# Kernel optimization log

Measured on AMD Instinct MI355X. Metric: run time of the kernel, lower is better.

The kernel has to match this reference:

```python
import jax, jax.numpy as jnp
import numpy as np

N_Q = 8          # number of residual quantizer stages
N_CODES = 1024   # 2 ** (75 // N_q + 1)
D = 128
GAMMA = 0.99


def setup_inputs() -> dict:
    key = jax.random.key(0)
    k1, k2, k3, k4 = jax.random.split(key, 4)
    data_object = jax.random.normal(k1, (16, D, 2048), dtype=jnp.float32)
    weights = jax.random.normal(k2, (N_Q, N_CODES, D), dtype=jnp.float32)
    # EMA cluster-size buffer; scale so most codes are 'alive' (>= 2)
    N_i = jax.random.uniform(k3, (N_Q, N_CODES), dtype=jnp.float32) * 100.0
    m_i = jax.random.normal(k4, (N_Q, N_CODES, D), dtype=jnp.float32)
    return {"data_object": data_object, "weights": weights, "N_i": N_i, "m_i": m_i}


def reference(data_object, weights, N_i, m_i):
    b, d, s = data_object.shape
    y = jnp.transpose(data_object, (0, 2, 1))  # [b, s, D]
    residual = y
    cur_y = jnp.zeros_like(y)
    all_idx, new_Ni, new_mi, new_W = [], [], [], []
    key = jax.random.key(42)
    one_m_g = 1.0 - GAMMA
    for i in range(N_Q):
        W = weights[i]  # [N, D]
        # squared euclidean distances: ||y||^2 + ||W||^2 - 2 y.W^T  -> [b, s, N]
        dist = ((residual ** 2).sum(-1)[..., None]
                + (W ** 2).sum(-1)[None, None, :]
                - 2.0 * jnp.einsum('bsd,nd->bsn', residual, W))
        idx = jnp.argmin(dist, axis=-1)          # [b, s]
        Q = W[idx]                               # gather  [b, s, D]
        cur_y = cur_y + Q
        flat_idx = idx.reshape(-1)               # [b*s]
        flat_res = residual.reshape(-1, d)       # [b*s, D]
        # fused scatter-reduce replacing the torch per-code mask loop
        counts = jax.ops.segment_sum(jnp.ones(flat_idx.shape, jnp.float32),
                                     flat_idx, num_segments=N_CODES)
        sums = jax.ops.segment_sum(flat_res, flat_idx, num_segments=N_CODES)
        Ni_new = N_i[i] * GAMMA + counts * one_m_g
        mi_new = m_i[i] * GAMMA + sums * one_m_g
        w_new = mi_new / jnp.clip(Ni_new, 1e-8)[:, None]
        # dead-code replacement with random residual vectors
        dead = Ni_new < 2.0
        rid = jax.random.randint(jax.random.fold_in(key, i), (N_CODES,),
                                 0, flat_res.shape[0])
        w_new = jnp.where(dead[:, None], flat_res[rid], w_new)
        all_idx.append(idx)
        new_Ni.append(Ni_new)
        new_mi.append(mi_new)
        new_W.append(w_new)
        residual = residual - Q
    cur_y_t = jnp.transpose(cur_y, (0, 2, 1))  # [b, D, s]
    # straight-through estimator
    logits = data_object + jax.lax.stop_gradient(cur_y_t - data_object)
    commitment_loss = jnp.mean((jax.lax.stop_gradient(cur_y_t) - data_object) ** 2)
    indices = jnp.stack(all_idx, axis=0)  # [N_q, b, s]
    return (logits, commitment_loss, indices,
            jnp.stack(new_Ni), jnp.stack(new_mi), jnp.stack(new_W))
```

## Files before the change

### kernel.cpp

```cpp
#include <hip/hip_runtime.h>
#include <hip/hip_bf16.h>

#define NQ 8
#define NC 1024
#define DD 128
#define BB 16
#define SS 2048
#define RR (BB * SS)
#define GAMMA_F 0.99f
#define TAU 0.03f

typedef __attribute__((ext_vector_type(8))) short bf16x8;
typedef __attribute__((ext_vector_type(4))) float f32x4;

typedef __attribute__((address_space(3))) void lds_void;
typedef const __attribute__((address_space(1))) void g1_void;
__device__ __forceinline__ void gload16(const void* g, void* l) {
  __builtin_amdgcn_global_load_lds((g1_void*)g, (lds_void*)l, 16, 0, 0);
}

__device__ __forceinline__ ushort f2bf(float x) {
  __hip_bfloat16 b = __float2bfloat16(x);
  return *reinterpret_cast<ushort*>(&b);
}
__device__ __forceinline__ float bf2f(ushort u) {
  unsigned v = ((unsigned)u) << 16;
  return *reinterpret_cast<float*>(&v);
}

__device__ __forceinline__ int swz(int r) {
  return ((r & 7) << 2) | ((r >> 3) & 1);
}

__global__ __launch_bounds__(256) void k_transpose_in(
    const float* __restrict__ data, float* __restrict__ res)
{
  __shared__ float tile[32][33];
  int b = blockIdx.z;
  int s0 = blockIdx.x << 5, d0 = blockIdx.y << 5;
  int tx = threadIdx.x, ty = threadIdx.y;
  #pragma unroll
  for (int r = 0; r < 32; r += 8)
    tile[ty + r][tx] = data[((size_t)b * DD + d0 + ty + r) * SS + s0 + tx];
  __syncthreads();
  #pragma unroll
  for (int r = 0; r < 32; r += 8)
    res[((size_t)b * SS + s0 + ty + r) * DD + d0 + tx] = tile[tx][ty + r];
}

__global__ void k_wsq(const float* __restrict__ W, float* __restrict__ wsq)
{
  int c = blockIdx.x * blockDim.x + threadIdx.x;
  if (c >= NQ * NC) return;
  const float4* p = reinterpret_cast<const float4*>(W + (size_t)c * DD);
  float s = 0.f;
  #pragma unroll 8
  for (int k = 0; k < DD / 4; ++k) {
    float4 v = p[k];
    s += v.x * v.x + v.y * v.y + v.z * v.z + v.w * v.w;
  }
  wsq[c] = s;
}

__global__ __launch_bounds__(256) void k_split(
    const float* __restrict__ src, ushort* __restrict__ dst)
{
  int fi = blockIdx.x * 256 + threadIdx.x;
  const float4* sp = reinterpret_cast<const float4*>(src) + (size_t)fi * 2;
  float4 a = sp[0], b = sp[1];
  ushort4 h0, h1, l0, l1;
  h0.x = f2bf(a.x); l0.x = f2bf(a.x - bf2f(h0.x));
  h0.y = f2bf(a.y); l0.y = f2bf(a.y - bf2f(h0.y));
  h0.z = f2bf(a.z); l0.z = f2bf(a.z - bf2f(h0.z));
  h0.w = f2bf(a.w); l0.w = f2bf(a.w - bf2f(h0.w));
  h1.x = f2bf(b.x); l1.x = f2bf(b.x - bf2f(h1.x));
  h1.y = f2bf(b.y); l1.y = f2bf(b.y - bf2f(h1.y));
  h1.z = f2bf(b.z); l1.z = f2bf(b.z - bf2f(h1.z));
  h1.w = f2bf(b.w); l1.w = f2bf(b.w - bf2f(h1.w));
  ushort4* dp = reinterpret_cast<ushort4*>(dst + (size_t)fi * 16);
  dp[0] = h0; dp[1] = h1; dp[2] = l0; dp[3] = l1;
}

__global__ __launch_bounds__(512, 2) void k_argmin(
    const ushort* __restrict__ res_hl, const ushort* __restrict__ w_hl,
    const float* __restrict__ wsq,
    int* __restrict__ idxw, float* __restrict__ idxf,
    int* __restrict__ count, int* __restrict__ fb_count,
    int* __restrict__ fb_list, int stage)
{
  __shared__ bf16x8 Bs[2][2048];
  __shared__ float Lm1[4][64], Lm2[4][64];
  __shared__ int   Li1[4][64];

  const int t = threadIdx.x;
  const int l = t & 63;
  const int w = t >> 6;
  const int wm = w >> 2;
  const int wn = w & 3;
  const int row0 = blockIdx.x * 64;
  const int l15 = l & 15, kg = l >> 4;
  const float* wsqs = wsq + stage * NC;

  bf16x8 ah[2][4], al[2][4];
  #pragma unroll
  for (int mf = 0; mf < 2; ++mf) {
    int r = row0 + wm * 32 + mf * 16 + l15;
    const bf16x8* rowp = reinterpret_cast<const bf16x8*>(res_hl + (size_t)r * 256);
    #pragma unroll
    for (int ks = 0; ks < 4; ++ks) {
      int ch = ks * 8 + kg * 2;
      ah[mf][ks] = rowp[ch];
      al[mf][ks] = rowp[ch + 1];
    }
  }

  #pragma unroll
  for (int it = 0; it < 4; ++it) {
    int fi = it * 512 + t;
    int cr = fi >> 5, sc = fi & 31;
    gload16(w_hl + ((size_t)(stage * NC + cr) * 32 + (sc ^ swz(cr))) * 8, &Bs[0][fi]);
  }
  #pragma unroll
  for (int it = 0; it < 4; ++it) {
    int fi = it * 512 + t;
    int cr = fi >> 5, sc = fi & 31;
    gload16(w_hl + ((size_t)(stage * NC + 64 + cr) * 32 + (sc ^ swz(cr))) * 8, &Bs[1][fi]);
  }

  float m1[2][4], m2[2][4];
  int i1[2][4];
  #pragma unroll
  for (int mf = 0; mf < 2; ++mf)
    #pragma unroll
    for (int rg = 0; rg < 4; ++rg) { m1[mf][rg] = 3.4e38f; m2[mf][rg] = 3.4e38f; i1[mf][rg] = 0; }

  for (int ct = 0; ct < 16; ++ct) {
    if (ct < 15) asm volatile("s_waitcnt vmcnt(4)" ::: "memory");
    else         asm volatile("s_waitcnt vmcnt(0)" ::: "memory");
    __builtin_amdgcn_sched_barrier(0);
    __builtin_amdgcn_s_barrier();

    const bf16x8* Bb = Bs[ct & 1];
    const int cr = wn * 16 + l15;

    f32x4 zero = {0.f, 0.f, 0.f, 0.f};
    f32x4 acc[2];
    acc[0] = zero; acc[1] = zero;

    #pragma unroll
    for (int ks = 0; ks < 4; ++ks) {
      const int ch = ks * 8 + kg * 2;
      bf16x8 bh = Bb[cr * 32 + (ch ^ swz(cr))];
      bf16x8 bl = Bb[cr * 32 + ((ch + 1) ^ swz(cr))];
      #pragma unroll
      for (int mf = 0; mf < 2; ++mf) {
        f32x4 cc = acc[mf];
        cc = __builtin_amdgcn_mfma_f32_16x16x32_bf16(ah[mf][ks], bh, cc, 0, 0, 0);
        cc = __builtin_amdgcn_mfma_f32_16x16x32_bf16(al[mf][ks], bh, cc, 0, 0, 0);
        cc = __builtin_amdgcn_mfma_f32_16x16x32_bf16(ah[mf][ks], bl, cc, 0, 0, 0);
        acc[mf] = cc;
      }
    }

    {
      int code = ct * 64 + wn * 16 + l15;
      float sq = wsqs[code];
      #pragma unroll
      for (int mf = 0; mf < 2; ++mf)
        #pragma unroll
        for (int rg = 0; rg < 4; ++rg) {
          float s = fmaf(-2.f, acc[mf][rg], sq);
          if (s < m1[mf][rg]) { m2[mf][rg] = m1[mf][rg]; m1[mf][rg] = s; i1[mf][rg] = code; }
          else if (s < m2[mf][rg]) m2[mf][rg] = s;
        }
    }

    __builtin_amdgcn_sched_barrier(0);
    __builtin_amdgcn_s_barrier();
    if (ct + 2 < 16) {
      bf16x8* dst = Bs[ct & 1];
      #pragma unroll
      for (int it = 0; it < 4; ++it) {
        int fi = it * 512 + t;
        int cr2 = fi >> 5, sc = fi & 31;
        gload16(w_hl + ((size_t)(stage * NC + (ct + 2) * 64 + cr2) * 32 + (sc ^ swz(cr2))) * 8,
                &dst[fi]);
      }
    }
  }

  #pragma unroll
  for (int mk = 1; mk <= 8; mk <<= 1) {
    #pragma unroll
    for (int mf = 0; mf < 2; ++mf)
      #pragma unroll
      for (int rg = 0; rg < 4; ++rg) {
        float om1 = __shfl_xor(m1[mf][rg], mk);
        int   oi  = __shfl_xor(i1[mf][rg], mk);
        float om2 = __shfl_xor(m2[mf][rg], mk);
        bool bwin = (om1 < m1[mf][rg]) || (om1 == m1[mf][rg] && oi < i1[mf][rg]);
        float lose = bwin ? m1[mf][rg] : om1;
        m2[mf][rg] = fminf(fminf(m2[mf][rg], om2), lose);
        if (bwin) { m1[mf][rg] = om1; i1[mf][rg] = oi; }
      }
  }
  if (l15 == 0) {
    #pragma unroll
    for (int mf = 0; mf < 2; ++mf)
      #pragma unroll
      for (int rg = 0; rg < 4; ++rg) {
        int rl = wm * 32 + mf * 16 + kg * 4 + rg;
        Lm1[wn][rl] = m1[mf][rg];
        Lm2[wn][rl] = m2[mf][rg];
        Li1[wn][rl] = i1[mf][rg];
      }
  }
  __syncthreads();

  if (t < 64) {
    float gm1 = Lm1[0][t], gm2 = Lm2[0][t];
    int gi = Li1[0][t];
    #pragma unroll
    for (int q = 1; q < 4; ++q) {
      float b1 = Lm1[q][t], b2 = Lm2[q][t];
      int bi = Li1[q][t];
      bool bwin = (b1 < gm1) || (b1 == gm1 && bi < gi);
      float lose = bwin ? gm1 : b1;
      gm2 = fminf(fminf(gm2, b2), lose);
      if (bwin) { gm1 = b1; gi = bi; }
    }
    int row = row0 + t;
    if (gm2 - gm1 > TAU) {
      idxw[row] = gi;
      idxf[row] = (float)gi;
      atomicAdd(&count[gi], 1);
    } else {
      int p = atomicAdd(fb_count, 1);
      fb_list[p] = row;
    }
  }
}

__global__ __launch_bounds__(256) void k_fallback(
    const float* __restrict__ res, const float* __restrict__ W,
    const float* __restrict__ wsq, const int* __restrict__ fb_count,
    const int* __restrict__ fb_list,
    int* __restrict__ idxw, float* __restrict__ idxf,
    int* __restrict__ count, int stage)
{
  __shared__ float rr[128];
  __shared__ float sv[256];
  __shared__ int   si[256];
  int n = *fb_count;
  int t = threadIdx.x;
  for (int b = blockIdx.x; b < n; b += gridDim.x) {
    int row = fb_list[b];
    __syncthreads();
    if (t < 128) rr[t] = res[(size_t)row * DD + t];
    __syncthreads();
    float bm = 3.4e38f; int bi = 0;
    #pragma unroll
    for (int j = 0; j < 4; ++j) {
      int c = t + j * 256;
      const float4* wp = reinterpret_cast<const float4*>(W + ((size_t)stage * NC + c) * DD);
      float dot = 0.f;
      #pragma unroll 8
      for (int k = 0; k < 32; ++k) {
        float4 wv = wp[k];
        dot = fmaf(rr[4 * k + 0], wv.x, dot);
        dot = fmaf(rr[4 * k + 1], wv.y, dot);
        dot = fmaf(rr[4 * k + 2], wv.z, dot);
        dot = fmaf(rr[4 * k + 3], wv.w, dot);
      }
      float s = fmaf(-2.f, dot, wsq[stage * NC + c]);
      if (s < bm || (s == bm && c < bi)) { bm = s; bi = c; }
    }
    sv[t] = bm; si[t] = bi;
    __syncthreads();
    for (int sft = 128; sft > 0; sft >>= 1) {
      if (t < sft) {
        float ov = sv[t + sft]; int oi = si[t + sft];
        if (ov < sv[t] || (ov == sv[t] && oi < si[t])) { sv[t] = ov; si[t] = oi; }
      }
      __syncthreads();
    }
    if (t == 0) {
      int win = si[0];
      idxw[row] = win;
      idxf[row] = (float)win;
      atomicAdd(&count[win], 1);
    }
  }
}

__global__ __launch_bounds__(1024) void k_scan(
    int* __restrict__ count, int* __restrict__ offs, int* __restrict__ pos)
{
  __shared__ int sc[1024];
  int t = threadIdx.x;
  sc[t] = count[t];
  __syncthreads();
  for (int off = 1; off < 1024; off <<= 1) {
    int v = (t >= off) ? sc[t - off] : 0;
    __syncthreads();
    sc[t] += v;
    __syncthreads();
  }
  offs[t + 1] = sc[t];
  if (t == 0) { offs[0] = 0; count[1024] = 0; }
  pos[t] = 0;
  count[t] = 0;
}

__global__ __launch_bounds__(256) void k_scatter(
    const int* __restrict__ idxw, const int* __restrict__ offs,
    int* __restrict__ pos, int* __restrict__ rows_sorted)
{
  int r = blockIdx.x * 256 + threadIdx.x;
  int c = idxw[r];
  int slot = offs[c] + atomicAdd(&pos[c], 1);
  rows_sorted[slot] = r;
}

__device__ __forceinline__ unsigned rotl32(unsigned v, int r) { return (v << r) | (v >> (32 - r)); }

__device__ void threefry2x32(unsigned ks0, unsigned ks1, unsigned x0, unsigned x1,
                             unsigned& o0, unsigned& o1)
{
  unsigned ks2 = ks0 ^ ks1 ^ 0x1BD11BDAu;
  x0 += ks0; x1 += ks1;
  x0 += x1; x1 = rotl32(x1, 13); x1 ^= x0;
  x0 += x1; x1 = rotl32(x1, 15); x1 ^= x0;
  x0 += x1; x1 = rotl32(x1, 26); x1 ^= x0;
  x0 += x1; x1 = rotl32(x1, 6);  x1 ^= x0;
  x0 += ks1; x1 += ks2 + 1u;
  x0 += x1; x1 = rotl32(x1, 17); x1 ^= x0;
  x0 += x1; x1 = rotl32(x1, 29); x1 ^= x0;
  x0 += x1; x1 = rotl32(x1, 16); x1 ^= x0;
  x0 += x1; x1 = rotl32(x1, 24); x1 ^= x0;
  x0 += ks2; x1 += ks0 + 2u;
  x0 += x1; x1 = rotl32(x1, 13); x1 ^= x0;
  x0 += x1; x1 = rotl32(x1, 15); x1 ^= x0;
  x0 += x1; x1 = rotl32(x1, 26); x1 ^= x0;
  x0 += x1; x1 = rotl32(x1, 6);  x1 ^= x0;
  x0 += ks0; x1 += ks1 + 3u;
  x0 += x1; x1 = rotl32(x1, 17); x1 ^= x0;
  x0 += x1; x1 = rotl32(x1, 29); x1 ^= x0;
  x0 += x1; x1 = rotl32(x1, 16); x1 ^= x0;
  x0 += x1; x1 = rotl32(x1, 24); x1 ^= x0;
  x0 += ks1; x1 += ks2 + 4u;
  x0 += x1; x1 = rotl32(x1, 13); x1 ^= x0;
  x0 += x1; x1 = rotl32(x1, 15); x1 ^= x0;
  x0 += x1; x1 = rotl32(x1, 26); x1 ^= x0;
  x0 += x1; x1 = rotl32(x1, 6);  x1 ^= x0;
  x0 += ks2; x1 += ks0 + 5u;
  o0 = x0; o1 = x1;
}

__global__ __launch_bounds__(1024) void k_finalize(
    const float* __restrict__ Ni_in, const float* __restrict__ mi_in,
    const int* __restrict__ offs, const int* __restrict__ rows_sorted,
    const float* __restrict__ res_cur,
    float* __restrict__ outNi, float* __restrict__ outmi, float* __restrict__ outW,
    int stage)
{
  __shared__ float red[8][128];
  const float ONEMG = (float)(1.0 - 0.99);
  int c = blockIdx.x;
  int t = threadIdx.x;
  int d = t & 127;
  int jw = t >> 7;
  int base = offs[c];
  int cnt = offs[c + 1] - base;
  const int* rs = rows_sorted + base;

  float sum = 0.f;
  int j = jw;
  for (; j + 24 < cnt; j += 32) {
    int r0 = rs[j];
    int r1 = rs[j + 8];
    int r2 = rs[j + 16];
    int r3 = rs[j + 24];
    float v0 = res_cur[(size_t)r0 * DD + d];
    float v1 = res_cur[(size_t)r1 * DD + d];
    float v2 = res_cur[(size_t)r2 * DD + d];
    float v3 = res_cur[(size_t)r3 * DD + d];
    sum += v0 + v1 + v2 + v3;
  }
  for (; j < cnt; j += 8)
    sum += res_cur[(size_t)rs[j] * DD + d];

  red[jw][d] = sum;
  __syncthreads();

  if (jw == 0) {
    float s = red[0][d] + red[1][d] + red[2][d] + red[3][d]
            + red[4][d] + red[5][d] + red[6][d] + red[7][d];
    float ni = Ni_in[stage * NC + c] * GAMMA_F + (float)cnt * ONEMG;
    float mm = mi_in[((size_t)stage * NC + c) * DD + d] * GAMMA_F + s * ONEMG;
    float w = mm / fmaxf(ni, 1e-8f);
    if (ni < 2.0f) {
      unsigned K0, K1, a0, a1, b0, b1, o0, o1;
      threefry2x32(0u, 42u, 0u, (unsigned)stage, K0, K1);
      threefry2x32(K0, K1, 0u, 2u, a0, a1);
      threefry2x32(K0, K1, 1u, 3u, b0, b1);
      unsigned bits;
      if (c < 512) { threefry2x32(a1, b1, (unsigned)c, (unsigned)(c + 512), o0, o1); bits = o0; }
      else         { threefry2x32(a1, b1, (unsigned)(c - 512), (unsigned)c, o0, o1); bits = o1; }
      int rid = (int)(bits & 32767u);
      w = res_cur[(size_t)rid * DD + d];
    }
    if (d == 0) outNi[stage * NC + c] = ni;
    size_t o = ((size_t)stage * NC + c) * DD + d;
    outmi[o] = mm;
    outW[o] = w;
  }
}

__global__ __launch_bounds__(256) void k_update(
    float* __restrict__ res, const float* __restrict__ W,
    const int* __restrict__ idx, ushort* __restrict__ res_hl, int stage)
{
  int row = blockIdx.x * 8 + (threadIdx.x >> 5);
  int d4 = threadIdx.x & 31;
  int id = idx[row];
  float4 r = reinterpret_cast<const float4*>(res + (size_t)row * DD)[d4];
  float4 q = reinterpret_cast<const float4*>(W + ((size_t)stage * NC + id) * DD)[d4];
  float4 o;
  o.x = r.x - q.x; o.y = r.y - q.y; o.z = r.z - q.z; o.w = r.w - q.w;
  reinterpret_cast<float4*>(res + (size_t)row * DD)[d4] = o;
  ushort4 hi, lo;
  hi.x = f2bf(o.x); lo.x = f2bf(o.x - bf2f(hi.x));
  hi.y = f2bf(o.y); lo.y = f2bf(o.y - bf2f(hi.y));
  hi.z = f2bf(o.z); lo.z = f2bf(o.z - bf2f(hi.z));
  hi.w = f2bf(o.w); lo.w = f2bf(o.w - bf2f(hi.w));
  size_t g = ((size_t)row * 16 + (d4 >> 1)) * 2;
  *reinterpret_cast<ushort4*>(res_hl + g * 8 + (d4 & 1) * 4) = hi;
  *reinterpret_cast<ushort4*>(res_hl + (g + 1) * 8 + (d4 & 1) * 4) = lo;
}

__global__ __launch_bounds__(256) void k_final(
    const float* __restrict__ data, const float* __restrict__ res,
    float* __restrict__ logits, float* __restrict__ partials)
{
  __shared__ float tile[32][33];
  __shared__ float wsum[4];
  int b = blockIdx.z, s0 = blockIdx.x << 5, d0 = blockIdx.y << 5;
  int tx = threadIdx.x, ty = threadIdx.y;
  #pragma unroll
  for (int r = 0; r < 32; r += 8)
    tile[ty + r][tx] = res[((size_t)b * SS + s0 + ty + r) * DD + d0 + tx];
  __syncthreads();
  float l = 0.f;
  #pragma unroll
  for (int r = 0; r < 32; r += 8) {
    int dv = d0 + ty + r, s = s0 + tx;
    size_t o = ((size_t)b * DD + dv) * SS + s;
    float rv = tile[tx][ty + r];
    logits[o] = data[o] - rv;
    l = fmaf(rv, rv, l);
  }
  #pragma unroll
  for (int m = 1; m < 64; m <<= 1) l += __shfl_xor(l, m);
  int lin = ty * 32 + tx;
  if ((lin & 63) == 0) wsum[lin >> 6] = l;
  __syncthreads();
  if (lin == 0) {
    int bl = (blockIdx.z * gridDim.y + blockIdx.y) * gridDim.x + blockIdx.x;
    partials[bl] = wsum[0] + wsum[1] + wsum[2] + wsum[3];
  }
}

__global__ __launch_bounds__(1024) void k_loss_reduce(
    const float* __restrict__ partials, float* __restrict__ loss)
{
  __shared__ float ws[16];
  int t = threadIdx.x;
  float s = partials[t] + partials[t + 1024] + partials[t + 2048] + partials[t + 3072];
  #pragma unroll
  for (int m = 1; m < 64; m <<= 1) s += __shfl_xor(s, m);
  if ((t & 63) == 0) ws[t >> 6] = s;
  __syncthreads();
  if (t < 16) {
    float v = ws[t];
    #pragma unroll
    for (int m = 1; m < 16; m <<= 1) v += __shfl_xor(v, m);
    if (t == 0) loss[0] = v * (1.0f / 4194304.0f);
  }
}

extern "C" void kernel_launch(void* const* d_in, const int* in_sizes, int n_in,
                              void* d_out, int out_size, void* d_ws, size_t ws_size,
                              hipStream_t stream)
{
  (void)in_sizes; (void)n_in; (void)out_size; (void)ws_size;
  const float* data = (const float*)d_in[0];
  const float* W    = (const float*)d_in[1];
  const float* Ni   = (const float*)d_in[2];
  const float* mi   = (const float*)d_in[3];

  float* out        = (float*)d_out;
  float* out_logits = out;
  float* out_loss   = out + (size_t)BB * DD * SS;
  float* out_idx    = out_loss + 1;
  float* out_Ni     = out_idx + (size_t)NQ * RR;
  float* out_mi     = out_Ni + (size_t)NQ * NC;
  float* out_W      = out_mi + (size_t)NQ * NC * DD;

  char* wp = (char*)d_ws;
  float*  resA        = (float*)wp;   wp += (size_t)RR * DD * 4;
  ushort* res_hl      = (ushort*)wp;  wp += (size_t)RR * DD * 4;
  ushort* w_hl        = (ushort*)wp;  wp += (size_t)NQ * NC * DD * 4;
  float*  wsq         = (float*)wp;   wp += (size_t)NQ * NC * 4;
  int*    idxw        = (int*)wp;     wp += (size_t)RR * 4;
  int*    fb_list     = (int*)wp;     wp += (size_t)RR * 4;
  int*    rows_sorted = (int*)wp;     wp += (size_t)RR * 4;
  int*    count       = (int*)wp;     wp += (size_t)1025 * 4;
  int*    fb_count    = count + 1024;
  int*    pos         = (int*)wp;     wp += (size_t)NC * 4;
  int*    offs        = (int*)wp;     wp += (size_t)(NC + 1) * 4;
  float*  partials    = (float*)wp;   wp += (size_t)4096 * 4;

  k_transpose_in<<<dim3(SS / 32, DD / 32, BB), dim3(32, 8), 0, stream>>>(data, resA);
  k_split<<<RR * 16 / 256, 256, 0, stream>>>(resA, res_hl);
  k_wsq<<<(NQ * NC + 255) / 256, 256, 0, stream>>>(W, wsq);
  k_split<<<NQ * NC * 16 / 256, 256, 0, stream>>>(W, w_hl);
  hipMemsetAsync(count, 0, 1025 * sizeof(int), stream);

  for (int i = 0; i < NQ; ++i) {
    k_argmin<<<RR / 64, 512, 0, stream>>>(res_hl, w_hl, wsq, idxw,
                                          out_idx + (size_t)i * RR,
                                          count, fb_count, fb_list, i);
    k_fallback<<<512, 256, 0, stream>>>(resA, W, wsq, fb_count, fb_list,
                                        idxw, out_idx + (size_t)i * RR, count, i);
    k_scan<<<1, 1024, 0, stream>>>(count, offs, pos);
    k_scatter<<<RR / 256, 256, 0, stream>>>(idxw, offs, pos, rows_sorted);
    k_finalize<<<NC, 1024, 0, stream>>>(Ni, mi, offs, rows_sorted, resA,
                                        out_Ni, out_mi, out_W, i);
    k_update<<<RR / 8, 256, 0, stream>>>(resA, W, idxw, res_hl, i);
  }

  k_final<<<dim3(SS / 32, DD / 32, BB), dim3(32, 8), 0, stream>>>(data, resA, out_logits, partials);
  k_loss_reduce<<<1, 1024, 0, stream>>>(partials, out_loss);
}
```

Before: 952.4 us.

## Pre-pack hi/lo bf16 operands in MFMA fragment order and drop LDS staging

The split and update kernels now write the bf16 hi/lo residual and codebook operands directly in the per-lane MFMA fragment layout. The argmin kernel then loads codebook fragments straight from global memory into registers with double-buffered register prefetch, dropping the shared-memory staging, swizzle, barriers and the cross-wave LDS reduction. Each wave now owns 16 rows and scans all 1024 codes, with 256-thread blocks. This removes LDS traffic and synchronisation, but every wave re-reads the full codebook from global memory or cache instead of sharing it through LDS.

```diff
diff --git a/kernel.cpp b/kernel.cpp
--- a/kernel.cpp
+++ b/kernel.cpp
@@ -13,12 +13,6 @@
 typedef __attribute__((ext_vector_type(8))) short bf16x8;
 typedef __attribute__((ext_vector_type(4))) float f32x4;
 
-typedef __attribute__((address_space(3))) void lds_void;
-typedef const __attribute__((address_space(1))) void g1_void;
-__device__ __forceinline__ void gload16(const void* g, void* l) {
-  __builtin_amdgcn_global_load_lds((g1_void*)g, (lds_void*)l, 16, 0, 0);
-}
-
 __device__ __forceinline__ ushort f2bf(float x) {
   __hip_bfloat16 b = __float2bfloat16(x);
   return *reinterpret_cast<ushort*>(&b);
@@ -26,10 +20,6 @@
 __device__ __forceinline__ float bf2f(ushort u) {
   unsigned v = ((unsigned)u) << 16;
   return *reinterpret_cast<float*>(&v);
-}
-
-__device__ __forceinline__ int swz(int r) {
-  return ((r & 7) << 2) | ((r >> 3) & 1);
 }
 
 __global__ __launch_bounds__(256) void k_transpose_in(
@@ -65,178 +55,123 @@
 __global__ __launch_bounds__(256) void k_split(
     const float* __restrict__ src, ushort* __restrict__ dst)
 {
-  int fi = blockIdx.x * 256 + threadIdx.x;
-  const float4* sp = reinterpret_cast<const float4*>(src) + (size_t)fi * 2;
-  float4 a = sp[0], b = sp[1];
-  ushort4 h0, h1, l0, l1;
-  h0.x = f2bf(a.x); l0.x = f2bf(a.x - bf2f(h0.x));
-  h0.y = f2bf(a.y); l0.y = f2bf(a.y - bf2f(h0.y));
-  h0.z = f2bf(a.z); l0.z = f2bf(a.z - bf2f(h0.z));
-  h0.w = f2bf(a.w); l0.w = f2bf(a.w - bf2f(h0.w));
-  h1.x = f2bf(b.x); l1.x = f2bf(b.x - bf2f(h1.x));
-  h1.y = f2bf(b.y); l1.y = f2bf(b.y - bf2f(h1.y));
-  h1.z = f2bf(b.z); l1.z = f2bf(b.z - bf2f(h1.z));
-  h1.w = f2bf(b.w); l1.w = f2bf(b.w - bf2f(h1.w));
-  ushort4* dp = reinterpret_cast<ushort4*>(dst + (size_t)fi * 16);
-  dp[0] = h0; dp[1] = h1; dp[2] = l0; dp[3] = l1;
-}
-
-__global__ __launch_bounds__(512, 2) void k_argmin(
+  int i = blockIdx.x * 256 + threadIdx.x;
+  int row = i >> 2, ks = i & 3;
+  const float4* sp = reinterpret_cast<const float4*>(src + (size_t)row * DD + ks * 32);
+  size_t gb = ((size_t)(row >> 4) * 8 + ks * 2) * 64 + (row & 15);
+  #pragma unroll
+  for (int kg = 0; kg < 4; ++kg) {
+    float4 a = sp[kg * 2], b = sp[kg * 2 + 1];
+    ushort4 h0, h1, l0, l1;
+    h0.x = f2bf(a.x); l0.x = f2bf(a.x - bf2f(h0.x));
+    h0.y = f2bf(a.y); l0.y = f2bf(a.y - bf2f(h0.y));
+    h0.z = f2bf(a.z); l0.z = f2bf(a.z - bf2f(h0.z));
+    h0.w = f2bf(a.w); l0.w = f2bf(a.w - bf2f(h0.w));
+    h1.x = f2bf(b.x); l1.x = f2bf(b.x - bf2f(h1.x));
+    h1.y = f2bf(b.y); l1.y = f2bf(b.y - bf2f(h1.y));
+    h1.z = f2bf(b.z); l1.z = f2bf(b.z - bf2f(h1.z));
+    h1.w = f2bf(b.w); l1.w = f2bf(b.w - bf2f(h1.w));
+    ushort* ph = dst + (gb + kg * 16) * 8;
+    *reinterpret_cast<ushort4*>(ph) = h0;
+    *reinterpret_cast<ushort4*>(ph + 4) = h1;
+    ushort* pl = ph + 64 * 8;
+    *reinterpret_cast<ushort4*>(pl) = l0;
+    *reinterpret_cast<ushort4*>(pl + 4) = l1;
+  }
+}
+
+__global__ __launch_bounds__(256, 3) void k_argmin(
     const ushort* __restrict__ res_hl, const ushort* __restrict__ w_hl,
     const float* __restrict__ wsq,
     int* __restrict__ idxw, float* __restrict__ idxf,
     int* __restrict__ count, int* __restrict__ fb_count,
     int* __restrict__ fb_list, int stage)
 {
-  __shared__ bf16x8 Bs[2][2048];
-  __shared__ float Lm1[4][64], Lm2[4][64];
-  __shared__ int   Li1[4][64];
-
   const int t = threadIdx.x;
   const int l = t & 63;
   const int w = t >> 6;
-  const int wm = w >> 2;
-  const int wn = w & 3;
+  const int l15 = l & 15;
   const int row0 = blockIdx.x * 64;
-  const int l15 = l & 15, kg = l >> 4;
   const float* wsqs = wsq + stage * NC;
-
-  bf16x8 ah[2][4], al[2][4];
-  #pragma unroll
-  for (int mf = 0; mf < 2; ++mf) {
-    int r = row0 + wm * 32 + mf * 16 + l15;
-    const bf16x8* rowp = reinterpret_cast<const bf16x8*>(res_hl + (size_t)r * 256);
-    #pragma unroll
-    for (int ks = 0; ks < 4; ++ks) {
-      int ch = ks * 8 + kg * 2;
-      ah[mf][ks] = rowp[ch];
-      al[mf][ks] = rowp[ch + 1];
-    }
-  }
-
-  #pragma unroll
-  for (int it = 0; it < 4; ++it) {
-    int fi = it * 512 + t;
-    int cr = fi >> 5, sc = fi & 31;
-    gload16(w_hl + ((size_t)(stage * NC + cr) * 32 + (sc ^ swz(cr))) * 8, &Bs[0][fi]);
-  }
-  #pragma unroll
-  for (int it = 0; it < 4; ++it) {
-    int fi = it * 512 + t;
-    int cr = fi >> 5, sc = fi & 31;
-    gload16(w_hl + ((size_t)(stage * NC + 64 + cr) * 32 + (sc ^ swz(cr))) * 8, &Bs[1][fi]);
-  }
-
-  float m1[2][4], m2[2][4];
-  int i1[2][4];
-  #pragma unroll
-  for (int mf = 0; mf < 2; ++mf)
-    #pragma unroll
-    for (int rg = 0; rg < 4; ++rg) { m1[mf][rg] = 3.4e38f; m2[mf][rg] = 3.4e38f; i1[mf][rg] = 0; }
-
-  for (int ct = 0; ct < 16; ++ct) {
-    if (ct < 15) asm volatile("s_waitcnt vmcnt(4)" ::: "memory");
-    else         asm volatile("s_waitcnt vmcnt(0)" ::: "memory");
-    __builtin_amdgcn_sched_barrier(0);
-    __builtin_amdgcn_s_barrier();
-
-    const bf16x8* Bb = Bs[ct & 1];
-    const int cr = wn * 16 + l15;
-
-    f32x4 zero = {0.f, 0.f, 0.f, 0.f};
-    f32x4 acc[2];
-    acc[0] = zero; acc[1] = zero;
-
-    #pragma unroll
-    for (int ks = 0; ks < 4; ++ks) {
-      const int ch = ks * 8 + kg * 2;
-      bf16x8 bh = Bb[cr * 32 + (ch ^ swz(cr))];
-      bf16x8 bl = Bb[cr * 32 + ((ch + 1) ^ swz(cr))];
-      #pragma unroll
-      for (int mf = 0; mf < 2; ++mf) {
-        f32x4 cc = acc[mf];
-        cc = __builtin_amdgcn_mfma_f32_16x16x32_bf16(ah[mf][ks], bh, cc, 0, 0, 0);
-        cc = __builtin_amdgcn_mfma_f32_16x16x32_bf16(al[mf][ks], bh, cc, 0, 0, 0);
-        cc = __builtin_amdgcn_mfma_f32_16x16x32_bf16(ah[mf][ks], bl, cc, 0, 0, 0);
-        acc[mf] = cc;
-      }
-    }
-
-    {
-      int code = ct * 64 + wn * 16 + l15;
-      float sq = wsqs[code];
-      #pragma unroll
-      for (int mf = 0; mf < 2; ++mf)
-        #pragma unroll
-        for (int rg = 0; rg < 4; ++rg) {
-          float s = fmaf(-2.f, acc[mf][rg], sq);
-          if (s < m1[mf][rg]) { m2[mf][rg] = m1[mf][rg]; m1[mf][rg] = s; i1[mf][rg] = code; }
-          else if (s < m2[mf][rg]) m2[mf][rg] = s;
-        }
-    }
-
-    __builtin_amdgcn_sched_barrier(0);
-    __builtin_amdgcn_s_barrier();
-    if (ct + 2 < 16) {
-      bf16x8* dst = Bs[ct & 1];
-      #pragma unroll
-      for (int it = 0; it < 4; ++it) {
-        int fi = it * 512 + t;
-        int cr2 = fi >> 5, sc = fi & 31;
-        gload16(w_hl + ((size_t)(stage * NC + (ct + 2) * 64 + cr2) * 32 + (sc ^ swz(cr2))) * 8,
-                &dst[fi]);
-      }
-    }
-  }
+  const ushort* wb = w_hl + (size_t)stage * NC * 256;
+
+  const size_t ab = ((size_t)(row0 >> 4) + w) * 8;
+  bf16x8 ah[4], al[4];
+  #pragma unroll
+  for (int ks = 0; ks < 4; ++ks) {
+    ah[ks] = *reinterpret_cast<const bf16x8*>(res_hl + ((ab + ks * 2) * 64 + l) * 8);
+    al[ks] = *reinterpret_cast<const bf16x8*>(res_hl + ((ab + ks * 2 + 1) * 64 + l) * 8);
+  }
+
+  float m1[4], m2[4];
+  int i1[4];
+  #pragma unroll
+  for (int rg = 0; rg < 4; ++rg) { m1[rg] = 3.4e38f; m2[rg] = 3.4e38f; i1[rg] = 0; }
+
+  bf16x8 bh0[4], bl0[4], bh1[4], bl1[4];
+
+#define LOADB(BH, BL, CT) {                                                       \
+    size_t bb = (size_t)(CT) * 8;                                                 \
+    _Pragma("unroll")                                                             \
+    for (int ks = 0; ks < 4; ++ks) {                                              \
+      BH[ks] = *reinterpret_cast<const bf16x8*>(wb + ((bb + ks * 2) * 64 + l) * 8);        \
+      BL[ks] = *reinterpret_cast<const bf16x8*>(wb + ((bb + ks * 2 + 1) * 64 + l) * 8);    \
+    } }
+
+#define COMPUTE(BH, BL, CT) {                                                     \
+    f32x4 accP = {0.f, 0.f, 0.f, 0.f};                                            \
+    f32x4 accQ = {0.f, 0.f, 0.f, 0.f};                                            \
+    _Pragma("unroll")                                                             \
+    for (int ks = 0; ks < 4; ++ks) {                                              \
+      accP = __builtin_amdgcn_mfma_f32_16x16x32_bf16(ah[ks], BH[ks], accP, 0, 0, 0); \
+      accQ = __builtin_amdgcn_mfma_f32_16x16x32_bf16(al[ks], BH[ks], accQ, 0, 0, 0); \
+      accQ = __builtin_amdgcn_mfma_f32_16x16x32_bf16(ah[ks], BL[ks], accQ, 0, 0, 0); \
+    }                                                                             \
+    int code = (CT) * 16 + l15;                                                   \
+    float sq = wsqs[code];                                                        \
+    _Pragma("unroll")                                                             \
+    for (int rg = 0; rg < 4; ++rg) {                                              \
+      float s = fmaf(-2.f, accP[rg] + accQ[rg], sq);                              \
+      if (s < m1[rg]) { m2[rg] = m1[rg]; m1[rg] = s; i1[rg] = code; }             \
+      else if (s < m2[rg]) m2[rg] = s;                                            \
+    } }
+
+  LOADB(bh0, bl0, 0);
+  for (int ct = 0; ct < 64; ct += 2) {
+    LOADB(bh1, bl1, ct + 1);
+    COMPUTE(bh0, bl0, ct);
+    if (ct + 2 < 64) LOADB(bh0, bl0, ct + 2);
+    COMPUTE(bh1, bl1, ct + 1);
+  }
+#undef LOADB
+#undef COMPUTE
 
   #pragma unroll
   for (int mk = 1; mk <= 8; mk <<= 1) {
     #pragma unroll
-    for (int mf = 0; mf < 2; ++mf)
-      #pragma unroll
-      for (int rg = 0; rg < 4; ++rg) {
-        float om1 = __shfl_xor(m1[mf][rg], mk);
-        int   oi  = __shfl_xor(i1[mf][rg], mk);
-        float om2 = __shfl_xor(m2[mf][rg], mk);
-        bool bwin = (om1 < m1[mf][rg]) || (om1 == m1[mf][rg] && oi < i1[mf][rg]);
-        float lose = bwin ? m1[mf][rg] : om1;
-        m2[mf][rg] = fminf(fminf(m2[mf][rg], om2), lose);
-        if (bwin) { m1[mf][rg] = om1; i1[mf][rg] = oi; }
+    for (int rg = 0; rg < 4; ++rg) {
+      float om1 = __shfl_xor(m1[rg], mk);
+      int   oi  = __shfl_xor(i1[rg], mk);
+      float om2 = __shfl_xor(m2[rg], mk);
+      bool bwin = (om1 < m1[rg]) || (om1 == m1[rg] && oi < i1[rg]);
+      float lose = bwin ? m1[rg] : om1;
+      m2[rg] = fminf(fminf(m2[rg], om2), lose);
+      if (bwin) { m1[rg] = om1; i1[rg] = oi; }
+    }
+  }
+  if (l15 == 0) {
+    int kg = l >> 4;
+    #pragma unroll
+    for (int rg = 0; rg < 4; ++rg) {
+      int row = row0 + w * 16 + kg * 4 + rg;
+      if (m2[rg] - m1[rg] > TAU) {
+        idxw[row] = i1[rg];
+        idxf[row] = (float)i1[rg];
+        atomicAdd(&count[i1[rg]], 1);
+      } else {
+        int p = atomicAdd(fb_count, 1);
+        fb_list[p] = row;
       }
-  }
-  if (l15 == 0) {
-    #pragma unroll
-    for (int mf = 0; mf < 2; ++mf)
-      #pragma unroll
-      for (int rg = 0; rg < 4; ++rg) {
-        int rl = wm * 32 + mf * 16 + kg * 4 + rg;
-        Lm1[wn][rl] = m1[mf][rg];
-        Lm2[wn][rl] = m2[mf][rg];
-        Li1[wn][rl] = i1[mf][rg];
-      }
-  }
-  __syncthreads();
-
-  if (t < 64) {
-    float gm1 = Lm1[0][t], gm2 = Lm2[0][t];
-    int gi = Li1[0][t];
-    #pragma unroll
-    for (int q = 1; q < 4; ++q) {
-      float b1 = Lm1[q][t], b2 = Lm2[q][t];
-      int bi = Li1[q][t];
-      bool bwin = (b1 < gm1) || (b1 == gm1 && bi < gi);
-      float lose = bwin ? gm1 : b1;
-      gm2 = fminf(fminf(gm2, b2), lose);
-      if (bwin) { gm1 = b1; gi = bi; }
-    }
-    int row = row0 + t;
-    if (gm2 - gm1 > TAU) {
-      idxw[row] = gi;
-      idxf[row] = (float)gi;
-      atomicAdd(&count[gi], 1);
-    } else {
-      int p = atomicAdd(fb_count, 1);
-      fb_list[p] = row;
     }
   }
 }
@@ -421,22 +356,35 @@
     float* __restrict__ res, const float* __restrict__ W,
     const int* __restrict__ idx, ushort* __restrict__ res_hl, int stage)
 {
-  int row = blockIdx.x * 8 + (threadIdx.x >> 5);
-  int d4 = threadIdx.x & 31;
+  int row = blockIdx.x * 16 + (threadIdx.x >> 4);
+  int g = threadIdx.x & 15;
   int id = idx[row];
-  float4 r = reinterpret_cast<const float4*>(res + (size_t)row * DD)[d4];
-  float4 q = reinterpret_cast<const float4*>(W + ((size_t)stage * NC + id) * DD)[d4];
-  float4 o;
-  o.x = r.x - q.x; o.y = r.y - q.y; o.z = r.z - q.z; o.w = r.w - q.w;
-  reinterpret_cast<float4*>(res + (size_t)row * DD)[d4] = o;
-  ushort4 hi, lo;
-  hi.x = f2bf(o.x); lo.x = f2bf(o.x - bf2f(hi.x));
-  hi.y = f2bf(o.y); lo.y = f2bf(o.y - bf2f(hi.y));
-  hi.z = f2bf(o.z); lo.z = f2bf(o.z - bf2f(hi.z));
-  hi.w = f2bf(o.w); lo.w = f2bf(o.w - bf2f(hi.w));
-  size_t g = ((size_t)row * 16 + (d4 >> 1)) * 2;
-  *reinterpret_cast<ushort4*>(res_hl + g * 8 + (d4 & 1) * 4) = hi;
-  *reinterpret_cast<ushort4*>(res_hl + (g + 1) * 8 + (d4 & 1) * 4) = lo;
+  const float4* rp = reinterpret_cast<const float4*>(res + (size_t)row * DD + g * 8);
+  const float4* qp = reinterpret_cast<const float4*>(W + ((size_t)stage * NC + id) * DD + g * 8);
+  float4 r0 = rp[0], r1 = rp[1];
+  float4 q0 = qp[0], q1 = qp[1];
+  float4 o0, o1;
+  o0.x = r0.x - q0.x; o0.y = r0.y - q0.y; o0.z = r0.z - q0.z; o0.w = r0.w - q0.w;
+  o1.x = r1.x - q1.x; o1.y = r1.y - q1.y; o1.z = r1.z - q1.z; o1.w = r1.w - q1.w;
+  float4* wp2 = reinterpret_cast<float4*>(res + (size_t)row * DD + g * 8);
+  wp2[0] = o0; wp2[1] = o1;
+  ushort4 h0, h1, l0, l1;
+  h0.x = f2bf(o0.x); l0.x = f2bf(o0.x - bf2f(h0.x));
+  h0.y = f2bf(o0.y); l0.y = f2bf(o0.y - bf2f(h0.y));
+  h0.z = f2bf(o0.z); l0.z = f2bf(o0.z - bf2f(h0.z));
+  h0.w = f2bf(o0.w); l0.w = f2bf(o0.w - bf2f(h0.w));
+  h1.x = f2bf(o1.x); l1.x = f2bf(o1.x - bf2f(h1.x));
+  h1.y = f2bf(o1.y); l1.y = f2bf(o1.y - bf2f(h1.y));
+  h1.z = f2bf(o1.z); l1.z = f2bf(o1.z - bf2f(h1.z));
+  h1.w = f2bf(o1.w); l1.w = f2bf(o1.w - bf2f(h1.w));
+  int ks = g >> 2, kg = g & 3;
+  size_t gb = ((size_t)(row >> 4) * 8 + ks * 2) * 64 + kg * 16 + (row & 15);
+  ushort* ph = res_hl + gb * 8;
+  *reinterpret_cast<ushort4*>(ph) = h0;
+  *reinterpret_cast<ushort4*>(ph + 4) = h1;
+  ushort* pl = ph + 64 * 8;
+  *reinterpret_cast<ushort4*>(pl) = l0;
+  *reinterpret_cast<ushort4*>(pl + 4) = l1;
 }
 
 __global__ __launch_bounds__(256) void k_final(
@@ -522,13 +470,13 @@
   float*  partials    = (float*)wp;   wp += (size_t)4096 * 4;
 
   k_transpose_in<<<dim3(SS / 32, DD / 32, BB), dim3(32, 8), 0, stream>>>(data, resA);
-  k_split<<<RR * 16 / 256, 256, 0, stream>>>(resA, res_hl);
+  k_split<<<RR * 4 / 256, 256, 0, stream>>>(resA, res_hl);
   k_wsq<<<(NQ * NC + 255) / 256, 256, 0, stream>>>(W, wsq);
-  k_split<<<NQ * NC * 16 / 256, 256, 0, stream>>>(W, w_hl);
+  k_split<<<NQ * NC * 4 / 256, 256, 0, stream>>>(W, w_hl);
   hipMemsetAsync(count, 0, 1025 * sizeof(int), stream);
 
   for (int i = 0; i < NQ; ++i) {
-    k_argmin<<<RR / 64, 512, 0, stream>>>(res_hl, w_hl, wsq, idxw,
+    k_argmin<<<RR / 64, 256, 0, stream>>>(res_hl, w_hl, wsq, idxw,
                                           out_idx + (size_t)i * RR,
                                           count, fb_count, fb_list, i);
     k_fallback<<<512, 256, 0, stream>>>(resA, W, wsq, fb_count, fb_list,
@@ -537,7 +485,7 @@
     k_scatter<<<RR / 256, 256, 0, stream>>>(idxw, offs, pos, rows_sorted);
     k_finalize<<<NC, 1024, 0, stream>>>(Ni, mi, offs, rows_sorted, resA,
                                         out_Ni, out_mi, out_W, i);
-    k_update<<<RR / 8, 256, 0, stream>>>(resA, W, idxw, res_hl, i);
+    k_update<<<RR / 16, 256, 0, stream>>>(resA, W, idxw, res_hl, i);
   }
 
   k_final<<<dim3(SS / 32, DD / 32, BB), dim3(32, 8), 0, stream>>>(data, resA, out_logits, partials);
```

After: 965.3 us. Within noise of the previous version (+1.4%).
